# Performance work log

Measured on AMD Instinct MI355X. Metric: run time of the kernel, lower is better.

Reference implementation:

```python
import jax, jax.numpy as jnp
import numpy as np

N_NODES = 100000
NEG_SLOPE = 0.2  # DGL GATConv default


def gat_layer(x, W, al, ar, src, dst):
    # x: [N, F_in], W: [F_in, H*D], al/ar: [H, D]
    H, D = al.shape
    f = (x @ W).reshape(-1, H, D)                      # [N, H, D]
    el = jnp.einsum('nhd,hd->nh', f, al)               # src attn term
    er = jnp.einsum('nhd,hd->nh', f, ar)               # dst attn term
    e = jax.nn.leaky_relu(el[src] + er[dst], NEG_SLOPE)  # [E, H]
    # segment softmax over incoming edges of each dst node
    m = jax.ops.segment_max(e, dst, num_segments=N_NODES)
    m = jnp.where(jnp.isfinite(m), m, jnp.zeros_like(m))  # isolated nodes -> -inf guard
    ex = jnp.exp(e - m[dst])                           # [E, H]
    s = jax.ops.segment_sum(ex, dst, num_segments=N_NODES)
    alpha = ex / (s[dst] + 1e-9)                       # [E, H]
    msg = f[src] * alpha[:, :, None]                   # [E, H, D]
    out = jax.ops.segment_sum(msg, dst, num_segments=N_NODES)  # [N, H, D]
    return out.reshape(N_NODES, H * D)


def setup_inputs() -> dict:
    key = jax.random.key(0)
    ks = jax.random.split(key, 12)
    x = jax.random.normal(ks[0], (N_NODES, 128), dtype=jnp.float32)
    edge_index = jax.random.randint(ks[1], (2, 1600000), 0, N_NODES, dtype=jnp.int32)
    sc = 0.05
    W0 = jax.random.normal(ks[2], (128, 128), dtype=jnp.float32) * sc
    al0 = jax.random.normal(ks[3], (4, 32), dtype=jnp.float32) * sc
    ar0 = jax.random.normal(ks[4], (4, 32), dtype=jnp.float32) * sc
    W1 = jax.random.normal(ks[5], (128, 128), dtype=jnp.float32) * sc
    al1 = jax.random.normal(ks[6], (4, 32), dtype=jnp.float32) * sc
    ar1 = jax.random.normal(ks[7], (4, 32), dtype=jnp.float32) * sc
    W2 = jax.random.normal(ks[8], (128, 128), dtype=jnp.float32) * sc
    al2 = jax.random.normal(ks[9], (4, 32), dtype=jnp.float32) * sc
    ar2 = jax.random.normal(ks[10], (4, 32), dtype=jnp.float32) * sc
    return {"x": x, "edge_index": edge_index,
            "W0": W0, "al0": al0, "ar0": ar0,
            "W1": W1, "al1": al1, "ar1": ar1,
            "W2": W2, "al2": al2, "ar2": ar2}


def reference(x, edge_index, W0, al0, ar0, W1, al1, ar1, W2, al2, ar2):
    src, dst = edge_index[0], edge_index[1]
    h = x
    for (W, al, ar) in ((W0, al0, ar0), (W1, al1, ar1), (W2, al2, ar2)):
        h = gat_layer(h, W, al, ar, src, dst)
        h = jax.nn.relu(h)  # dropout_rate = 0.0 -> identity
    return h
```

## Files before the change

kernel.cpp:

```cpp
#include <hip/hip_runtime.h>
#include <math.h>

#define NEG_SLOPE 0.2f
#define NBUCK 512
#define BHCHUNK 8192
#define BCHUNK 4096

typedef __attribute__((ext_vector_type(8))) short short8;
typedef __attribute__((ext_vector_type(4))) float f32x4;

__device__ __forceinline__ unsigned short bf16rne(float x) {
    unsigned u = __float_as_uint(x);
    u += 0x7fffu + ((u >> 16) & 1u);
    return (unsigned short)(u >> 16);
}
__device__ __forceinline__ unsigned pack_bf2(float x, float y) {
    unsigned ux = __float_as_uint(x), uy = __float_as_uint(y);
    ux = (ux + 0x7fffu + ((ux >> 16) & 1u)) >> 16;
    uy = (uy + 0x7fffu + ((uy >> 16) & 1u)) & 0xffff0000u;
    return ux | uy;
}

__global__ __launch_bounds__(256) void k_front(
    const int* __restrict__ dst, int* __restrict__ bcnt, int E,
    const float4* __restrict__ x, uint4* __restrict__ Xb, int n8,
    const float* __restrict__ w0, const float* __restrict__ w1,
    const float* __restrict__ w2, unsigned short* __restrict__ Wt,
    int nbB, int nbCvt) {
    __shared__ int cnt[NBUCK];
    int bb = blockIdx.x, t = threadIdx.x;
    if (bb < nbB) {
        for (int i = t; i < NBUCK; i += 256) cnt[i] = 0;
        __syncthreads();
        int e0 = bb * BHCHUNK;
        int n = min(BHCHUNK, E - e0);
        for (int i = t; i < n; i += 256) atomicAdd(&cnt[dst[e0 + i] >> 8], 1);
        __syncthreads();
        for (int i = t; i < NBUCK; i += 256)
            if (cnt[i]) atomicAdd(&bcnt[i], cnt[i]);
    } else if (bb < nbB + nbCvt) {
        int id = (bb - nbB) * 256 + t;
        if (id < n8) {
            float4 a = x[id * 2], b = x[id * 2 + 1];
            uint4 o;
            o.x = pack_bf2(a.x, a.y);
            o.y = pack_bf2(a.z, a.w);
            o.z = pack_bf2(b.x, b.y);
            o.w = pack_bf2(b.z, b.w);
            Xb[id] = o;
        }
    } else {
        int id = (bb - nbB - nbCvt) * 256 + t;
        int layer = id >> 14, rem = id & 16383;
        int k = rem >> 7, n = rem & 127;
        const float* W = (layer == 0) ? w0 : (layer == 1) ? w1 : w2;
        Wt[layer * 16384 + n * 128 + k] = bf16rne(W[k * 128 + n]);
    }
}

__global__ void k_bscan(const int* __restrict__ bcnt, int* __restrict__ bbase,
                        int* __restrict__ bcur, int* __restrict__ rowstart,
                        int N, int E) {
    __shared__ int sd[NBUCK];
    int t = threadIdx.x;
    int c = bcnt[t];
    sd[t] = c;
    __syncthreads();
    for (int s = 1; s < NBUCK; s <<= 1) {
        int x = (t >= s) ? sd[t - s] : 0;
        __syncthreads();
        sd[t] += x;
        __syncthreads();
    }
    int excl = sd[t] - c;
    bbase[t] = excl;
    bcur[t] = excl;
    if (t == NBUCK - 1) bbase[NBUCK] = excl + c;
    if (t == 0) rowstart[N] = E;
}

__global__ __launch_bounds__(256) void k_bin(
    const int* __restrict__ src, const int* __restrict__ dst,
    int* __restrict__ bcur, unsigned* __restrict__ packed, int E) {
    __shared__ int cnt[NBUCK];
    __shared__ int gbase[NBUCK];
    for (int i = threadIdx.x; i < NBUCK; i += 256) cnt[i] = 0;
    __syncthreads();
    int e0 = blockIdx.x * BCHUNK;
    int n = min(BCHUNK, E - e0);
    for (int i = threadIdx.x; i < n; i += 256)
        atomicAdd(&cnt[dst[e0 + i] >> 8], 1);
    __syncthreads();
    for (int i = threadIdx.x; i < NBUCK; i += 256) {
        int c = cnt[i];
        gbase[i] = c ? atomicAdd(&bcur[i], c) : 0;
        cnt[i] = 0;
    }
    __syncthreads();
    for (int i = threadIdx.x; i < n; i += 256) {
        int d = dst[e0 + i];
        int b = d >> 8;
        int o = atomicAdd(&cnt[b], 1);
        packed[gbase[b] + o] = ((unsigned)src[e0 + i] << 8) | (unsigned)(d & 255);
    }
}

__global__ __launch_bounds__(256) void k_place2(
    const unsigned* __restrict__ packed, const int* __restrict__ bbase,
    int* __restrict__ rowstart, unsigned* __restrict__ cpack, int N) {
    __shared__ int cnt[256], sd[256], lcur[256];
    int b = blockIdx.x, t = threadIdx.x;
    int base = bbase[b], end = bbase[b + 1];
    cnt[t] = 0;
    __syncthreads();
    for (int i = base + t; i < end; i += 256)
        atomicAdd(&cnt[packed[i] & 255u], 1);
    __syncthreads();
    sd[t] = cnt[t];
    __syncthreads();
    for (int s = 1; s < 256; s <<= 1) {
        int x = (t >= s) ? sd[t - s] : 0;
        __syncthreads();
        sd[t] += x;
        __syncthreads();
    }
    int excl = sd[t] - cnt[t];
    int gid = (b << 8) + t;
    if (gid < N) rowstart[gid] = base + excl;
    lcur[t] = base + excl;
    __syncthreads();
    for (int i = base + t; i < end; i += 256) {
        unsigned p = packed[i];
        unsigned dl = p & 255u;
        int pos = atomicAdd(&lcur[dl], 1);
        cpack[pos] = (dl << 17) | (p >> 8);
    }
}

__global__ __launch_bounds__(256) void k_gemm(
    const unsigned short* __restrict__ Ab,
    const unsigned short* __restrict__ Wt,
    const float* __restrict__ alv, const float* __restrict__ arv,
    unsigned short* __restrict__ Fb,
    float* __restrict__ el, float* __restrict__ er, int M) {
    __shared__ unsigned short cst[4][32][128];
    int t = threadIdx.x;
    int wv = t >> 6, l = t & 63;
    int l15 = l & 15, quad = l >> 4;
    int row0 = blockIdx.x * 128 + wv * 32;

    f32x4 acc[2][8];
#pragma unroll
    for (int mi = 0; mi < 2; mi++)
#pragma unroll
        for (int nt = 0; nt < 8; nt++)
            acc[mi][nt] = (f32x4){0.f, 0.f, 0.f, 0.f};

    int rA0 = min(row0 + l15, M - 1);
    int rA1 = min(row0 + 16 + l15, M - 1);
    const uint4* pA0 = (const uint4*)(Ab + (size_t)rA0 * 128) + quad;
    const uint4* pA1 = (const uint4*)(Ab + (size_t)rA1 * 128) + quad;
    const uint4* pW = (const uint4*)Wt;

#pragma unroll
    for (int ks = 0; ks < 4; ks++) {
        union { uint4 u; short8 s; } a0, a1, b[8];
        a0.u = pA0[ks * 4];
        a1.u = pA1[ks * 4];
#pragma unroll
        for (int nt = 0; nt < 8; nt++)
            b[nt].u = pW[(nt * 16 + l15) * 16 + quad + ks * 4];
#pragma unroll
        for (int nt = 0; nt < 8; nt++) {
            acc[0][nt] = __builtin_amdgcn_mfma_f32_16x16x32_bf16(a0.s, b[nt].s, acc[0][nt], 0, 0, 0);
            acc[1][nt] = __builtin_amdgcn_mfma_f32_16x16x32_bf16(a1.s, b[nt].s, acc[1][nt], 0, 0, 0);
        }
    }

#pragma unroll
    for (int mi = 0; mi < 2; mi++)
#pragma unroll
        for (int nt = 0; nt < 8; nt++)
#pragma unroll
            for (int r = 0; r < 4; r++)
                cst[wv][mi * 16 + quad * 4 + r][nt * 16 + l15] = bf16rne(acc[mi][nt][r]);

    int rrow = l >> 1;
    int cb = (l & 1) * 64;
    int grow = row0 + rrow;
    bool ok = grow < M;
    float pe[2] = {0.f, 0.f}, pr[2] = {0.f, 0.f};
#pragma unroll
    for (int i = 0; i < 8; i++) {
        uint4 v = *(const uint4*)&cst[wv][rrow][cb + i * 8];
        if (ok) ((uint4*)(Fb + (size_t)grow * 128 + cb))[i] = v;
        int hi = i >> 2;
        int c0 = cb + i * 8;
        unsigned uu[4] = {v.x, v.y, v.z, v.w};
#pragma unroll
        for (int q = 0; q < 4; q++) {
            float fa = __uint_as_float(uu[q] << 16);
            float fb = __uint_as_float(uu[q] & 0xffff0000u);
            pe[hi] += fa * alv[c0 + 2 * q] + fb * alv[c0 + 2 * q + 1];
            pr[hi] += fa * arv[c0 + 2 * q] + fb * arv[c0 + 2 * q + 1];
        }
    }
    float qe0 = __shfl_xor(pe[0], 1, 64), qe1 = __shfl_xor(pe[1], 1, 64);
    float qr0 = __shfl_xor(pr[0], 1, 64), qr1 = __shfl_xor(pr[1], 1, 64);
    if (((l & 1) == 0) && ok) {
        *(float4*)&el[(size_t)grow * 4] = make_float4(pe[0], pe[1], qe0, qe1);
        *(float4*)&er[(size_t)grow * 4] = make_float4(pr[0], pr[1], qr0, qr1);
    }
}

template <int OUT_BF16>
__global__ __launch_bounds__(256) void k_aggr(
    const int* __restrict__ rowstart, const unsigned* __restrict__ cpack,
    const float* __restrict__ el, const float* __restrict__ er,
    const uint4* __restrict__ F4, void* __restrict__ outp, int N, int E) {
    int lane = threadIdx.x & 63;
    int sub = lane >> 4;
    int l16 = lane & 15;
    int w = blockIdx.x * 16 + ((threadIdx.x >> 6) << 2) + sub;
    bool active = w < N;
    int wc = active ? w : N - 1;
    int start = rowstart[wc];
    int dg = active ? (rowstart[wc + 1] - start) : 0;
    int h = l16 >> 2;
    float rr = er[(size_t)wc * 4 + h];

    float s_acc = 0.f;
    float a0 = 0.f, a1 = 0.f, a2 = 0.f, a3 = 0.f;
    float a4 = 0.f, a5 = 0.f, a6 = 0.f, a7 = 0.f;

    int ncc = (dg + 3) >> 2;
    int m = max(ncc, __shfl_xor(ncc, 16, 64));
    int nccmax = max(m, __shfl_xor(m, 32, 64));
    int full = dg >> 2;
    int mf = min(full, __shfl_xor(full, 16, 64));
    int minfull = min(mf, __shfl_xor(mf, 32, 64));

    auto loadc = [&](int c, uint4* fb, float* eb) {
        int j = c << 2;
        if (c < minfull) {
#pragma unroll
            for (int u = 0; u < 4; u++) {
                int e = start + j + u;
                int s = (int)(cpack[e] & 0x1ffffu);
                fb[u] = F4[(size_t)s * 16 + l16];
                eb[u] = el[(size_t)s * 4 + h];
            }
        } else {
#pragma unroll
            for (int u = 0; u < 4; u++) {
                int jj = j + u;
                int e = min(max(start + min(jj, dg - 1), 0), E - 1);
                int s = (int)(cpack[e] & 0x1ffffu);
                fb[u] = F4[(size_t)s * 16 + l16];
                float ev = el[(size_t)s * 4 + h];
                eb[u] = (jj < dg) ? ev : -1e30f;
            }
        }
    };
    auto consume = [&](const uint4* fb, const float* eb) {
#pragma unroll
        for (int u = 0; u < 4; u++) {
            float e = eb[u] + rr;
            e = fmaxf(e, NEG_SLOPE * e);
            float p = __expf(e);
            s_acc += p;
            a0 += p * __uint_as_float(fb[u].x << 16);
            a1 += p * __uint_as_float(fb[u].x & 0xffff0000u);
            a2 += p * __uint_as_float(fb[u].y << 16);
            a3 += p * __uint_as_float(fb[u].y & 0xffff0000u);
            a4 += p * __uint_as_float(fb[u].z << 16);
            a5 += p * __uint_as_float(fb[u].z & 0xffff0000u);
            a6 += p * __uint_as_float(fb[u].w << 16);
            a7 += p * __uint_as_float(fb[u].w & 0xffff0000u);
        }
    };

    uint4 f0[4], f1[4];
    float e0[4], e1[4];
    if (nccmax > 0) {
        loadc(0, f0, e0);
        for (int c = 1; c < nccmax; c++) {
            if (c & 1) { loadc(c, f1, e1); consume(f0, e0); }
            else       { loadc(c, f0, e0); consume(f1, e1); }
        }
        if (nccmax & 1) consume(f0, e0); else consume(f1, e1);
    }

    if (!active) return;
    float inv = 1.f / (s_acc + 1e-9f);
    a0 = fmaxf(a0 * inv, 0.f); a1 = fmaxf(a1 * inv, 0.f);
    a2 = fmaxf(a2 * inv, 0.f); a3 = fmaxf(a3 * inv, 0.f);
    a4 = fmaxf(a4 * inv, 0.f); a5 = fmaxf(a5 * inv, 0.f);
    a6 = fmaxf(a6 * inv, 0.f); a7 = fmaxf(a7 * inv, 0.f);
    if (OUT_BF16) {
        uint4 pk;
        pk.x = pack_bf2(a0, a1);
        pk.y = pack_bf2(a2, a3);
        pk.z = pack_bf2(a4, a5);
        pk.w = pack_bf2(a6, a7);
        ((uint4*)outp)[(size_t)w * 16 + l16] = pk;
    } else {
        float4* op = (float4*)outp + (size_t)w * 32 + l16 * 2;
        op[0] = make_float4(a0, a1, a2, a3);
        op[1] = make_float4(a4, a5, a6, a7);
    }
}


extern "C" void kernel_launch(void* const* d_in, const int* in_sizes, int n_in,
                              void* d_out, int out_size, void* d_ws, size_t ws_size,
                              hipStream_t stream) {
    const float* x = (const float*)d_in[0];
    const int* ei = (const int*)d_in[1];
    int N = in_sizes[0] / 128;
    int E = in_sizes[1] / 2;
    const int* src = ei;
    const int* dst = ei + E;
    const float* Wm[3] = {(const float*)d_in[2], (const float*)d_in[5], (const float*)d_in[8]};
    const float* al[3] = {(const float*)d_in[3], (const float*)d_in[6], (const float*)d_in[9]};
    const float* ar[3] = {(const float*)d_in[4], (const float*)d_in[7], (const float*)d_in[10]};

    char* p = (char*)d_ws;
    auto carve = [&](size_t bytes) {
        char* r = p;
        p += (bytes + 255) & ~(size_t)255;
        return r;
    };
    unsigned short* Xb = (unsigned short*)carve((size_t)N * 128 * 2);
    unsigned short* Hb = (unsigned short*)carve((size_t)N * 128 * 2);
    unsigned short* Fb = (unsigned short*)carve((size_t)N * 128 * 2);
    unsigned short* Wt = (unsigned short*)carve((size_t)3 * 16384 * 2);
    float* el       = (float*)carve((size_t)N * 4 * 4);
    float* er       = (float*)carve((size_t)N * 4 * 4);
    int* rowstart   = (int*)carve((size_t)(N + 1) * 4);
    unsigned* cpack = (unsigned*)carve((size_t)E * 4);
    unsigned* packed= (unsigned*)carve((size_t)E * 4);
    int* bcnt       = (int*)carve((size_t)NBUCK * 4);
    int* bbase      = (int*)carve((size_t)(NBUCK + 1) * 4);
    int* bcur       = (int*)carve((size_t)NBUCK * 4);

    int NBUSED = (N + 255) >> 8;

    hipMemsetAsync(bcnt, 0, NBUCK * 4, stream);
    int nbB = (E + BHCHUNK - 1) / BHCHUNK;
    int n8 = N * 128 / 8;
    int nbCvt = (n8 + 255) / 256;
    int nbPrep = (3 * 16384) / 256;
    k_front<<<nbB + nbCvt + nbPrep, 256, 0, stream>>>(
        dst, bcnt, E, (const float4*)x, (uint4*)Xb, n8,
        Wm[0], Wm[1], Wm[2], Wt, nbB, nbCvt);
    k_bscan<<<1, NBUCK, 0, stream>>>(bcnt, bbase, bcur, rowstart, N, E);
    k_bin<<<(E + BCHUNK - 1) / BCHUNK, 256, 0, stream>>>(src, dst, bcur, packed, E);
    k_place2<<<NBUSED, 256, 0, stream>>>(packed, bbase, rowstart, cpack, N);

    int gb = (N + 127) / 128;
    int ab = (N + 15) / 16;
    k_gemm<<<gb, 256, 0, stream>>>(Xb, Wt, al[0], ar[0], Fb, el, er, N);
    k_aggr<1><<<ab, 256, 0, stream>>>(rowstart, cpack, el, er, (const uint4*)Fb, Hb, N, E);

    k_gemm<<<gb, 256, 0, stream>>>(Hb, Wt + 16384, al[1], ar[1], Fb, el, er, N);
    k_aggr<1><<<ab, 256, 0, stream>>>(rowstart, cpack, el, er, (const uint4*)Fb, Hb, N, E);

    k_gemm<<<gb, 256, 0, stream>>>(Hb, Wt + 32768, al[2], ar[2], Fb, el, er, N);
    k_aggr<0><<<ab, 256, 0, stream>>>(rowstart, cpack, el, er, (const uint4*)Fb, d_out, N, E);
}
```

Baseline: 503.8 us.

## Fuse aggregation with next layer's GEMM and attention projections

Adds a kernel that aggregates 128 destination rows per block, keeps the bf16 results in shared memory, and then runs the next layer's MFMA GEMM and el/er projection on them. This removes two launches and the global write and re-read of the intermediate hidden features between layers. Ping-pong el/er and feature buffers are added so a layer never reads what it is writing. The trade-off is lower parallelism: each wave now handles 32 rows serially through the gather loop, with 8x fewer blocks than the standalone aggregation, which could reduce latency hiding on the memory-bound gather.

```diff
diff --git a/kernel.cpp b/kernel.cpp
--- a/kernel.cpp
+++ b/kernel.cpp
@@ -213,6 +213,166 @@
     }
 }
 
+__global__ __launch_bounds__(256) void k_fused(
+    const int* __restrict__ rowstart, const unsigned* __restrict__ cpack,
+    const float* __restrict__ el_in, const float* __restrict__ er_in,
+    const uint4* __restrict__ F4,
+    const unsigned short* __restrict__ Wt,
+    const float* __restrict__ alv, const float* __restrict__ arv,
+    unsigned short* __restrict__ Fb_out,
+    float* __restrict__ el_out, float* __restrict__ er_out, int N, int E) {
+    __shared__ unsigned short cst[4][32][128];
+    int t = threadIdx.x;
+    int wv = t >> 6, lane = t & 63;
+    int sub = lane >> 4;
+    int l16 = lane & 15;
+    int h = l16 >> 2;
+    int row0 = blockIdx.x * 128 + wv * 32;
+
+    for (int ro = 0; ro < 8; ro++) {
+        int i = ro * 4 + sub;
+        int w = row0 + i;
+        bool active = w < N;
+        int wc = active ? w : N - 1;
+        int start = rowstart[wc];
+        int dg = active ? (rowstart[wc + 1] - start) : 0;
+        float rr = er_in[(size_t)wc * 4 + h];
+
+        float s_acc = 0.f;
+        float a0 = 0.f, a1 = 0.f, a2 = 0.f, a3 = 0.f;
+        float a4 = 0.f, a5 = 0.f, a6 = 0.f, a7 = 0.f;
+
+        int ncc = (dg + 3) >> 2;
+        int mm = max(ncc, __shfl_xor(ncc, 16, 64));
+        int nccmax = max(mm, __shfl_xor(mm, 32, 64));
+        int full = dg >> 2;
+        int mf = min(full, __shfl_xor(full, 16, 64));
+        int minfull = min(mf, __shfl_xor(mf, 32, 64));
+
+        auto loadc = [&](int c, uint4* fb, float* eb) {
+            int j = c << 2;
+            if (c < minfull) {
+#pragma unroll
+                for (int u = 0; u < 4; u++) {
+                    int e = start + j + u;
+                    int s = (int)(cpack[e] & 0x1ffffu);
+                    fb[u] = F4[(size_t)s * 16 + l16];
+                    eb[u] = el_in[(size_t)s * 4 + h];
+                }
+            } else {
+#pragma unroll
+                for (int u = 0; u < 4; u++) {
+                    int jj = j + u;
+                    int e = min(max(start + min(jj, dg - 1), 0), E - 1);
+                    int s = (int)(cpack[e] & 0x1ffffu);
+                    fb[u] = F4[(size_t)s * 16 + l16];
+                    float ev = el_in[(size_t)s * 4 + h];
+                    eb[u] = (jj < dg) ? ev : -1e30f;
+                }
+            }
+        };
+        auto consume = [&](const uint4* fb, const float* eb) {
+#pragma unroll
+            for (int u = 0; u < 4; u++) {
+                float e = eb[u] + rr;
+                e = fmaxf(e, NEG_SLOPE * e);
+                float p = __expf(e);
+                s_acc += p;
+                a0 += p * __uint_as_float(fb[u].x << 16);
+                a1 += p * __uint_as_float(fb[u].x & 0xffff0000u);
+                a2 += p * __uint_as_float(fb[u].y << 16);
+                a3 += p * __uint_as_float(fb[u].y & 0xffff0000u);
+                a4 += p * __uint_as_float(fb[u].z << 16);
+                a5 += p * __uint_as_float(fb[u].z & 0xffff0000u);
+                a6 += p * __uint_as_float(fb[u].w << 16);
+                a7 += p * __uint_as_float(fb[u].w & 0xffff0000u);
+            }
+        };
+
+        uint4 f0[4], f1[4];
+        float e0[4], e1[4];
+        if (nccmax > 0) {
+            loadc(0, f0, e0);
+            for (int c = 1; c < nccmax; c++) {
+                if (c & 1) { loadc(c, f1, e1); consume(f0, e0); }
+                else       { loadc(c, f0, e0); consume(f1, e1); }
+            }
+            if (nccmax & 1) consume(f0, e0); else consume(f1, e1);
+        }
+
+        float inv = active ? 1.f / (s_acc + 1e-9f) : 0.f;
+        a0 = fmaxf(a0 * inv, 0.f); a1 = fmaxf(a1 * inv, 0.f);
+        a2 = fmaxf(a2 * inv, 0.f); a3 = fmaxf(a3 * inv, 0.f);
+        a4 = fmaxf(a4 * inv, 0.f); a5 = fmaxf(a5 * inv, 0.f);
+        a6 = fmaxf(a6 * inv, 0.f); a7 = fmaxf(a7 * inv, 0.f);
+        uint4 pk;
+        pk.x = pack_bf2(a0, a1);
+        pk.y = pack_bf2(a2, a3);
+        pk.z = pack_bf2(a4, a5);
+        pk.w = pack_bf2(a6, a7);
+        *(uint4*)&cst[wv][i][l16 * 8] = pk;
+    }
+
+    f32x4 acc[2][8];
+#pragma unroll
+    for (int mi = 0; mi < 2; mi++)
+#pragma unroll
+        for (int nt = 0; nt < 8; nt++)
+            acc[mi][nt] = (f32x4){0.f, 0.f, 0.f, 0.f};
+
+    const uint4* pW = (const uint4*)Wt;
+#pragma unroll
+    for (int ks = 0; ks < 4; ks++) {
+        union { uint4 u; short8 s; } av0, av1, b[8];
+        av0.u = *(const uint4*)&cst[wv][l16][sub * 8 + ks * 32];
+        av1.u = *(const uint4*)&cst[wv][16 + l16][sub * 8 + ks * 32];
+#pragma unroll
+        for (int nt = 0; nt < 8; nt++)
+            b[nt].u = pW[(nt * 16 + l16) * 16 + sub + ks * 4];
+#pragma unroll
+        for (int nt = 0; nt < 8; nt++) {
+            acc[0][nt] = __builtin_amdgcn_mfma_f32_16x16x32_bf16(av0.s, b[nt].s, acc[0][nt], 0, 0, 0);
+            acc[1][nt] = __builtin_amdgcn_mfma_f32_16x16x32_bf16(av1.s, b[nt].s, acc[1][nt], 0, 0, 0);
+        }
+    }
+
+    __syncthreads();
+#pragma unroll
+    for (int mi = 0; mi < 2; mi++)
+#pragma unroll
+        for (int nt = 0; nt < 8; nt++)
+#pragma unroll
+            for (int r = 0; r < 4; r++)
+                cst[wv][mi * 16 + sub * 4 + r][nt * 16 + l16] = bf16rne(acc[mi][nt][r]);
+
+    int rrow = lane >> 1;
+    int cb = (lane & 1) * 64;
+    int grow = row0 + rrow;
+    bool ok = grow < N;
+    float pe[2] = {0.f, 0.f}, pr[2] = {0.f, 0.f};
+#pragma unroll
+    for (int i = 0; i < 8; i++) {
+        uint4 v = *(const uint4*)&cst[wv][rrow][cb + i * 8];
+        if (ok) ((uint4*)(Fb_out + (size_t)grow * 128 + cb))[i] = v;
+        int hi = i >> 2;
+        int c0 = cb + i * 8;
+        unsigned uu[4] = {v.x, v.y, v.z, v.w};
+#pragma unroll
+        for (int q = 0; q < 4; q++) {
+            float fa = __uint_as_float(uu[q] << 16);
+            float fb = __uint_as_float(uu[q] & 0xffff0000u);
+            pe[hi] += fa * alv[c0 + 2 * q] + fb * alv[c0 + 2 * q + 1];
+            pr[hi] += fa * arv[c0 + 2 * q] + fb * arv[c0 + 2 * q + 1];
+        }
+    }
+    float qe0 = __shfl_xor(pe[0], 1, 64), qe1 = __shfl_xor(pe[1], 1, 64);
+    float qr0 = __shfl_xor(pr[0], 1, 64), qr1 = __shfl_xor(pr[1], 1, 64);
+    if (((lane & 1) == 0) && ok) {
+        *(float4*)&el_out[(size_t)grow * 4] = make_float4(pe[0], pe[1], qe0, qe1);
+        *(float4*)&er_out[(size_t)grow * 4] = make_float4(pr[0], pr[1], qr0, qr1);
+    }
+}
+
 template <int OUT_BF16>
 __global__ __launch_bounds__(256) void k_aggr(
     const int* __restrict__ rowstart, const unsigned* __restrict__ cpack,
@@ -221,12 +381,12 @@
     int lane = threadIdx.x & 63;
     int sub = lane >> 4;
     int l16 = lane & 15;
+    int h = l16 >> 2;
     int w = blockIdx.x * 16 + ((threadIdx.x >> 6) << 2) + sub;
     bool active = w < N;
     int wc = active ? w : N - 1;
     int start = rowstart[wc];
     int dg = active ? (rowstart[wc + 1] - start) : 0;
-    int h = l16 >> 2;
     float rr = er[(size_t)wc * 4 + h];
 
     float s_acc = 0.f;
@@ -332,11 +492,13 @@
         return r;
     };
     unsigned short* Xb = (unsigned short*)carve((size_t)N * 128 * 2);
+    unsigned short* Fb = (unsigned short*)carve((size_t)N * 128 * 2);
     unsigned short* Hb = (unsigned short*)carve((size_t)N * 128 * 2);
-    unsigned short* Fb = (unsigned short*)carve((size_t)N * 128 * 2);
     unsigned short* Wt = (unsigned short*)carve((size_t)3 * 16384 * 2);
     float* el       = (float*)carve((size_t)N * 4 * 4);
     float* er       = (float*)carve((size_t)N * 4 * 4);
+    float* el2      = (float*)carve((size_t)N * 4 * 4);
+    float* er2      = (float*)carve((size_t)N * 4 * 4);
     int* rowstart   = (int*)carve((size_t)(N + 1) * 4);
     unsigned* cpack = (unsigned*)carve((size_t)E * 4);
     unsigned* packed= (unsigned*)carve((size_t)E * 4);
@@ -361,11 +523,10 @@
     int gb = (N + 127) / 128;
     int ab = (N + 15) / 16;
     k_gemm<<<gb, 256, 0, stream>>>(Xb, Wt, al[0], ar[0], Fb, el, er, N);
-    k_aggr<1><<<ab, 256, 0, stream>>>(rowstart, cpack, el, er, (const uint4*)Fb, Hb, N, E);
-
-    k_gemm<<<gb, 256, 0, stream>>>(Hb, Wt + 16384, al[1], ar[1], Fb, el, er, N);
-    k_aggr<1><<<ab, 256, 0, stream>>>(rowstart, cpack, el, er, (const uint4*)Fb, Hb, N, E);
-
-    k_gemm<<<gb, 256, 0, stream>>>(Hb, Wt + 32768, al[2], ar[2], Fb, el, er, N);
-    k_aggr<0><<<ab, 256, 0, stream>>>(rowstart, cpack, el, er, (const uint4*)Fb, d_out, N, E);
-}
+    k_fused<<<gb, 256, 0, stream>>>(rowstart, cpack, el, er, (const uint4*)Fb,
+                                    Wt + 16384, al[1], ar[1], Hb, el2, er2, N, E);
+    k_fused<<<gb, 256, 0, stream>>>(rowstart, cpack, el2, er2, (const uint4*)Hb,
+                                    Wt + 32768, al[2], ar[2], Fb, el, er, N, E);
+    k_aggr<0><<<ab, 256, 0, stream>>>(rowstart, cpack, el, er, (const uint4*)Fb,
+                                      d_out, N, E);
+}
```

Result: slower. 547.0 us (+8.6%).
